# Performance work log

Hardware: AMD Instinct MI355X
Metric: run time of the kernel (lower is better)

The kernel has to match this reference:

```python
import jax, jax.numpy as jnp
import numpy as np

NP, P, H, NB = 14, 16, 12, 6  # n_patches per side, patch size, heads, blocks
HD, EMB, SEQ = 64, 768, NP * NP + 1


def _layernorm(x, g, b, eps=1e-5):
    m = x.mean(axis=-1, keepdims=True)
    v = x.var(axis=-1, keepdims=True)
    return (x - m) * jax.lax.rsqrt(v + eps) * g + b


def setup_inputs() -> dict:
    key = jax.random.key(0)
    ks = jax.random.split(key, 16)
    s = 0.02
    B = 64
    inp = {
        "images": jax.random.normal(ks[0], (B, 3, 224, 224), jnp.float32),
        "Wmap": jax.random.normal(ks[1], (768, 768), jnp.float32) * s,
        "bmap": jnp.zeros((768,), jnp.float32),
        "cls_tok": jax.random.normal(ks[2], (1, 768), jnp.float32) * s,
        "pos": jax.random.normal(ks[3], (SEQ, 768), jnp.float32) * s,
        "ln1_g": jnp.ones((NB, 768), jnp.float32),
        "ln1_b": jnp.zeros((NB, 768), jnp.float32),
        "Wq": jax.random.normal(ks[4], (NB, H, HD, HD), jnp.float32) * s,
        "bq": jnp.zeros((NB, H, HD), jnp.float32),
        "Wk": jax.random.normal(ks[5], (NB, H, HD, HD), jnp.float32) * s,
        "bk": jnp.zeros((NB, H, HD), jnp.float32),
        "Wv": jax.random.normal(ks[6], (NB, H, HD, HD), jnp.float32) * s,
        "bv": jnp.zeros((NB, H, HD), jnp.float32),
        "ln2_g": jnp.ones((NB, 768), jnp.float32),
        "ln2_b": jnp.zeros((NB, 768), jnp.float32),
        "W1": jax.random.normal(ks[7], (NB, 768, 3072), jnp.float32) * s,
        "b1": jnp.zeros((NB, 3072), jnp.float32),
        "W2": jax.random.normal(ks[8], (NB, 3072, 768), jnp.float32) * s,
        "b2": jnp.zeros((NB, 768), jnp.float32),
        "Whead": jax.random.normal(ks[9], (768, 10), jnp.float32) * s,
        "bhead": jnp.zeros((10,), jnp.float32),
    }
    return inp


def reference(images, Wmap, bmap, cls_tok, pos, ln1_g, ln1_b, Wq, bq, Wk, bk,
              Wv, bv, ln2_g, ln2_b, W1, b1, W2, b2, Whead, bhead):
    B = images.shape[0]
    # patchify: (B,3,224,224) -> (B,196,768); per-patch channel-first flatten
    x = images.reshape(B, 3, NP, P, NP, P)
    x = x.transpose(0, 2, 4, 1, 3, 5).reshape(B, NP * NP, 3 * P * P)
    tokens = x @ Wmap + bmap  # (B,196,768)
    tokens = jnp.concatenate(
        [jnp.broadcast_to(cls_tok[None], (B, 1, EMB)), tokens], axis=1)
    out = tokens + pos[None]  # (B,197,768)
    scale = 1.0 / jnp.sqrt(jnp.asarray(H, out.dtype))  # NOTE: source divides by sqrt(num_heads)
    for i in range(NB):
        h = _layernorm(out, ln1_g[i], ln1_b[i])
        xh = h.reshape(B, SEQ, H, HD)
        q = jnp.einsum('bshd,hde->bshe', xh, Wq[i]) + bq[i]
        k = jnp.einsum('bshd,hde->bshe', xh, Wk[i]) + bk[i]
        v = jnp.einsum('bshd,hde->bshe', xh, Wv[i]) + bv[i]
        attn = jax.nn.softmax(
            jnp.einsum('bqhd,bkhd->bhqk', q, k) * scale, axis=-1)
        o = jnp.einsum('bhqk,bkhd->bqhd', attn, v).reshape(B, SEQ, EMB)
        out = out + o
        h2 = _layernorm(out, ln2_g[i], ln2_b[i])
        mlp = jax.nn.gelu(h2 @ W1[i] + b1[i], approximate=False) @ W2[i] + b2[i]
        out = out + mlp
    cls = out[:, 0]  # (B,768)
    return jax.nn.softmax(cls @ Whead + bhead, axis=-1)
```

## Files before the change

### kernel.cpp

```cpp
#include <hip/hip_runtime.h>
#include <cstddef>

#define BATCH 64
#define SEQL  197
#define EMB   768
#define NH    12
#define HDIM  64
#define NBLK  6
#define MLPD  3072
#define TOKS  12608
#define PTOK  12544
#define ATT_SCALE 0.28867513459481287f
#define LOG2E 1.4426950408889634f

typedef short bf16x8 __attribute__((ext_vector_type(8)));
typedef float f32x4  __attribute__((ext_vector_type(4)));

__device__ inline float bf2f(unsigned short u) {
  union { unsigned int i; float f; } c; c.i = ((unsigned int)u) << 16; return c.f;
}
__device__ inline unsigned short f2bf(float f) {
  union { float f; unsigned int i; } c; c.f = f;
  unsigned int r = c.i + 0x7FFFu + ((c.i >> 16) & 1u);
  return (unsigned short)(r >> 16);
}

__device__ __forceinline__ float gelu_f(float x) {
  float u = __builtin_fabsf(x) * 0.70710678118654752f;
  float t = __builtin_amdgcn_rcpf(__builtin_fmaf(0.3275911f, u, 1.0f));
  float p = __builtin_fmaf(1.061405429f, t, -1.453152027f);
  p = __builtin_fmaf(p, t, 1.421413741f);
  p = __builtin_fmaf(p, t, -0.284496736f);
  p = __builtin_fmaf(p, t, 0.254829592f);
  p = p * t;
  float e = __expf(-u * u);
  float er = __builtin_fmaf(-p, e, 1.0f);
  er = __builtin_copysignf(er, x);
  return 0.5f * x * (1.0f + er);
}

__device__ __forceinline__ void gload16(const unsigned short* g, void* l) {
  __builtin_amdgcn_global_load_lds(
      (const __attribute__((address_space(1))) unsigned int*)g,
      (__attribute__((address_space(3))) unsigned int*)l, 16, 0, 0);
}

__global__ __launch_bounds__(256) void patchify_kernel(const float* __restrict__ img,
                                                       unsigned short* __restrict__ out) {
  int i4 = blockIdx.x * 256 + threadIdx.x;
  int f4 = i4 % 192;
  int r  = i4 / 192;
  int b  = r / 196, t = r - b * 196;
  int f  = f4 * 4;
  int c  = f >> 8;
  int rem = f & 255;
  int iy = rem >> 4, ix = rem & 15;
  int py = t / 14, px = t - py * 14;
  const float* src = img + ((((size_t)b * 3 + c) * 224 + py * 16 + iy) * 224 + px * 16 + ix);
  float4 v = *(const float4*)src;
  ushort4 u;
  u.x = f2bf(v.x); u.y = f2bf(v.y); u.z = f2bf(v.z); u.w = f2bf(v.w);
  *(ushort4*)(out + (size_t)r * 768 + f) = u;
}

__global__ __launch_bounds__(256) void clspos_kernel(const float* __restrict__ cls,
                                                     const float* __restrict__ pos,
                                                     float* __restrict__ X) {
  int idx = blockIdx.x * 256 + threadIdx.x;
  int b = idx / 768, e = idx - b * 768;
  X[(size_t)b * SEQL * 768 + e] = cls[e] + pos[e];
}

__global__ __launch_bounds__(256) void wconv_kernel(const float* __restrict__ W,
                                                    unsigned short* __restrict__ Wt,
                                                    int K, int N, int perm) {
  __shared__ float t[32][33];
  int k0 = blockIdx.x * 32, n0 = blockIdx.y * 32;
  int kk = threadIdx.x >> 3, nn = (threadIdx.x & 7) * 4;
  float4 v = *(const float4*)&W[(size_t)(k0 + kk) * N + n0 + nn];
  t[nn + 0][kk] = v.x; t[nn + 1][kk] = v.y; t[nn + 2][kk] = v.z; t[nn + 3][kk] = v.w;
  __syncthreads();
  int nr = threadIdx.x >> 3, kc = (threadIdx.x & 7) * 4;
  ushort4 u;
  u.x = f2bf(t[nr][kc + 0]); u.y = f2bf(t[nr][kc + 1]);
  u.z = f2bf(t[nr][kc + 2]); u.w = f2bf(t[nr][kc + 3]);
  if (!perm) {
    *(ushort4*)&Wt[(size_t)(n0 + nr) * K + k0 + kc] = u;
  } else {
    size_t base = (size_t)(n0 + nr) * K + (size_t)(k0 & ~63);
    int klo = (k0 & 32) + kc;
    size_t st = base + (size_t)((klo & 15) * 4 + (klo >> 4));
    Wt[st + 0]  = u.x;
    Wt[st + 4]  = u.y;
    Wt[st + 8]  = u.z;
    Wt[st + 12] = u.w;
  }
}

__global__ __launch_bounds__(256) void qwconv_kernel(const float* __restrict__ Wq,
                                                     const float* __restrict__ Wk,
                                                     const float* __restrict__ Wv,
                                                     unsigned short* __restrict__ Wt) {
  int mh = blockIdx.x;
  int m = mh / 12, h = mh - m * 12;
  const float* src = (m == 0 ? Wq : (m == 1 ? Wk : Wv)) + (size_t)h * 4096;
  unsigned short* dst = Wt + (size_t)mh * 4096;
  for (int idx = threadIdx.x; idx < 4096; idx += 256) {
    int d = idx >> 6, e = idx & 63;
    dst[e * 64 + d] = f2bf(src[idx]);
  }
}

template<int MODE>
__global__ __launch_bounds__(256) void gemm_mfma(const unsigned short* __restrict__ A, int lda,
                                                 const unsigned short* __restrict__ Bt, int ldb,
                                                 void* __restrict__ Cv,
                                                 const float* __restrict__ bias,
                                                 const float* __restrict__ pos,
                                                 int M, int N, int K) {
  __shared__ short As[8192];
  __shared__ short Bs[8192];
  const int tid  = threadIdx.x;
  const int wid  = tid >> 6, lane = tid & 63;
  const int wr   = wid >> 1, wc = wid & 1;
  const int fr   = lane & 15;
  const int fq   = lane >> 4;
  const int m0   = blockIdx.y * 128;
  const int n0   = blockIdx.x * 128;
  const int srow = lane >> 3;
  const int schk = lane & 7;
  const int Mc   = M - 1;

  const unsigned short* ap[4];
  const unsigned short* bp[4];
  char* al[4];
  char* bl[4];
#pragma unroll
  for (int i = 0; i < 4; ++i) {
    int row = i * 32 + wid * 8 + srow;
    int gr = m0 + row; if (gr > Mc) gr = Mc;
    int sw = (schk ^ (row & 7)) << 3;
    ap[i] = A + (size_t)gr * lda + sw;
    bp[i] = Bt + (size_t)(n0 + row) * ldb + sw;
    al[i] = (char*)As + i * 4096 + wid * 1024;
    bl[i] = (char*)Bs + i * 4096 + wid * 1024;
  }

  f32x4 acc[4][4];
#pragma unroll
  for (int m = 0; m < 4; ++m)
#pragma unroll
    for (int n = 0; n < 4; ++n) acc[m][n] = (f32x4)0.f;

  const int T = K >> 6;
  for (int t = 0; t < T; ++t) {
#pragma unroll
    for (int i = 0; i < 4; ++i) {
      gload16(ap[i], al[i]);
      gload16(bp[i], bl[i]);
      ap[i] += 64;
      bp[i] += 64;
    }
    __syncthreads();
#pragma unroll
    for (int ks = 0; ks < 2; ++ks) {
      bf16x8 af[4], bfr[4];
#pragma unroll
      for (int m = 0; m < 4; ++m) {
        int row = (wr << 6) + (m << 4) + fr;
        int ch = ((ks << 2) + fq) ^ (row & 7);
        af[m] = *(const bf16x8*)&As[(row << 6) + (ch << 3)];
      }
#pragma unroll
      for (int n = 0; n < 4; ++n) {
        int row = (wc << 6) + (n << 4) + fr;
        int ch = ((ks << 2) + fq) ^ (row & 7);
        bfr[n] = *(const bf16x8*)&Bs[(row << 6) + (ch << 3)];
      }
#pragma unroll
      for (int m = 0; m < 4; ++m)
#pragma unroll
        for (int n = 0; n < 4; ++n)
          acc[m][n] = __builtin_amdgcn_mfma_f32_16x16x32_bf16(af[m], bfr[n], acc[m][n], 0, 0, 0);
    }
    __syncthreads();
  }

#pragma unroll
  for (int m = 0; m < 4; ++m) {
#pragma unroll
    for (int j = 0; j < 4; ++j) {
      int r = m0 + (wr << 6) + (m << 4) + (fq << 2) + j;
      if (r >= M) continue;
      if (MODE == 1) {
        ushort4 q;
        float v0 = acc[m][0][j] + bias[n0 + (wc << 6) + 0 * 16 + fr];
        float v1 = acc[m][1][j] + bias[n0 + (wc << 6) + 1 * 16 + fr];
        float v2 = acc[m][2][j] + bias[n0 + (wc << 6) + 2 * 16 + fr];
        float v3 = acc[m][3][j] + bias[n0 + (wc << 6) + 3 * 16 + fr];
        q.x = f2bf(gelu_f(v0));
        q.y = f2bf(gelu_f(v1));
        q.z = f2bf(gelu_f(v2));
        q.w = f2bf(gelu_f(v3));
        *(ushort4*)&((unsigned short*)Cv)[(size_t)r * MLPD + n0 + (wc << 6) + fr * 4] = q;
      } else {
#pragma unroll
        for (int n = 0; n < 4; ++n) {
          int c = n0 + (wc << 6) + (n << 4) + fr;
          float v = acc[m][n][j] + bias[c];
          if (MODE == 0) {
            int b = r / 196, t = r - b * 196;
            ((float*)Cv)[((size_t)b * SEQL + 1 + t) * 768 + c] = v + pos[(size_t)(1 + t) * 768 + c];
          } else {
            ((float*)Cv)[(size_t)r * 768 + c] += v;
          }
        }
      }
    }
  }
}

__global__ __launch_bounds__(256) void ln_kernel(const float* __restrict__ Xi,
                                                 unsigned short* __restrict__ Ho,
                                                 const float* __restrict__ g,
                                                 const float* __restrict__ bb) {
  int tok = blockIdx.x * 4 + (threadIdx.x >> 6);
  int lane = threadIdx.x & 63;
  const float* x = Xi + (size_t)tok * 768;
  float4 v0 = *(const float4*)(x + lane * 4);
  float4 v1 = *(const float4*)(x + 256 + lane * 4);
  float4 v2 = *(const float4*)(x + 512 + lane * 4);
  float s = v0.x + v0.y + v0.z + v0.w + v1.x + v1.y + v1.z + v1.w + v2.x + v2.y + v2.z + v2.w;
  float q = v0.x*v0.x + v0.y*v0.y + v0.z*v0.z + v0.w*v0.w
          + v1.x*v1.x + v1.y*v1.y + v1.z*v1.z + v1.w*v1.w
          + v2.x*v2.x + v2.y*v2.y + v2.z*v2.z + v2.w*v2.w;
#pragma unroll
  for (int o = 32; o > 0; o >>= 1) { s += __shfl_xor(s, o); q += __shfl_xor(q, o); }
  float mean = s * (1.f / 768.f);
  float var  = q * (1.f / 768.f) - mean * mean;
  float rs = rsqrtf(var + 1e-5f);
  unsigned short* outp = Ho + (size_t)tok * 768;
  float4 g0 = *(const float4*)(g + lane * 4);
  float4 g1 = *(const float4*)(g + 256 + lane * 4);
  float4 g2 = *(const float4*)(g + 512 + lane * 4);
  float4 b0 = *(const float4*)(bb + lane * 4);
  float4 b1 = *(const float4*)(bb + 256 + lane * 4);
  float4 b2 = *(const float4*)(bb + 512 + lane * 4);
  ushort4 s0, s1, s2;
  s0.x = f2bf((v0.x - mean) * rs * g0.x + b0.x); s0.y = f2bf((v0.y - mean) * rs * g0.y + b0.y);
  s0.z = f2bf((v0.z - mean) * rs * g0.z + b0.z); s0.w = f2bf((v0.w - mean) * rs * g0.w + b0.w);
  s1.x = f2bf((v1.x - mean) * rs * g1.x + b1.x); s1.y = f2bf((v1.y - mean) * rs * g1.y + b1.y);
  s1.z = f2bf((v1.z - mean) * rs * g1.z + b1.z); s1.w = f2bf((v1.w - mean) * rs * g1.w + b1.w);
  s2.x = f2bf((v2.x - mean) * rs * g2.x + b2.x); s2.y = f2bf((v2.y - mean) * rs * g2.y + b2.y);
  s2.z = f2bf((v2.z - mean) * rs * g2.z + b2.z); s2.w = f2bf((v2.w - mean) * rs * g2.w + b2.w);
  *(ushort4*)(outp + lane * 4) = s0;
  *(ushort4*)(outp + 256 + lane * 4) = s1;
  *(ushort4*)(outp + 512 + lane * 4) = s2;
}

__global__ __launch_bounds__(256) void ln_res_kernel(float* __restrict__ X,
                                                     const unsigned short* __restrict__ O,
                                                     unsigned short* __restrict__ Ho,
                                                     const float* __restrict__ g,
                                                     const float* __restrict__ bb) {
  int tok = blockIdx.x * 4 + (threadIdx.x >> 6);
  int lane = threadIdx.x & 63;
  float* x = X + (size_t)tok * 768;
  const unsigned short* op = O + (size_t)tok * 768;
  float4 v0 = *(const float4*)(x + lane * 4);
  float4 v1 = *(const float4*)(x + 256 + lane * 4);
  float4 v2 = *(const float4*)(x + 512 + lane * 4);
  ushort4 o0 = *(const ushort4*)(op + lane * 4);
  ushort4 o1 = *(const ushort4*)(op + 256 + lane * 4);
  ushort4 o2 = *(const ushort4*)(op + 512 + lane * 4);
  v0.x += bf2f(o0.x); v0.y += bf2f(o0.y); v0.z += bf2f(o0.z); v0.w += bf2f(o0.w);
  v1.x += bf2f(o1.x); v1.y += bf2f(o1.y); v1.z += bf2f(o1.z); v1.w += bf2f(o1.w);
  v2.x += bf2f(o2.x); v2.y += bf2f(o2.y); v2.z += bf2f(o2.z); v2.w += bf2f(o2.w);
  *(float4*)(x + lane * 4) = v0;
  *(float4*)(x + 256 + lane * 4) = v1;
  *(float4*)(x + 512 + lane * 4) = v2;
  float s = v0.x + v0.y + v0.z + v0.w + v1.x + v1.y + v1.z + v1.w + v2.x + v2.y + v2.z + v2.w;
  float q = v0.x*v0.x + v0.y*v0.y + v0.z*v0.z + v0.w*v0.w
          + v1.x*v1.x + v1.y*v1.y + v1.z*v1.z + v1.w*v1.w
          + v2.x*v2.x + v2.y*v2.y + v2.z*v2.z + v2.w*v2.w;
#pragma unroll
  for (int o = 32; o > 0; o >>= 1) { s += __shfl_xor(s, o); q += __shfl_xor(q, o); }
  float mean = s * (1.f / 768.f);
  float var  = q * (1.f / 768.f) - mean * mean;
  float rs = rsqrtf(var + 1e-5f);
  unsigned short* outp = Ho + (size_t)tok * 768;
  float4 g0 = *(const float4*)(g + lane * 4);
  float4 g1 = *(const float4*)(g + 256 + lane * 4);
  float4 g2 = *(const float4*)(g + 512 + lane * 4);
  float4 b0 = *(const float4*)(bb + lane * 4);
  float4 b1 = *(const float4*)(bb + 256 + lane * 4);
  float4 b2 = *(const float4*)(bb + 512 + lane * 4);
  ushort4 s0, s1, s2;
  s0.x = f2bf((v0.x - mean) * rs * g0.x + b0.x); s0.y = f2bf((v0.y - mean) * rs * g0.y + b0.y);
  s0.z = f2bf((v0.z - mean) * rs * g0.z + b0.z); s0.w = f2bf((v0.w - mean) * rs * g0.w + b0.w);
  s1.x = f2bf((v1.x - mean) * rs * g1.x + b1.x); s1.y = f2bf((v1.y - mean) * rs * g1.y + b1.y);
  s1.z = f2bf((v1.z - mean) * rs * g1.z + b1.z); s1.w = f2bf((v1.w - mean) * rs * g1.w + b1.w);
  s2.x = f2bf((v2.x - mean) * rs * g2.x + b2.x); s2.y = f2bf((v2.y - mean) * rs * g2.y + b2.y);
  s2.z = f2bf((v2.z - mean) * rs * g2.z + b2.z); s2.w = f2bf((v2.w - mean) * rs * g2.w + b2.w);
  *(ushort4*)(outp + lane * 4) = s0;
  *(ushort4*)(outp + 256 + lane * 4) = s1;
  *(ushort4*)(outp + 512 + lane * 4) = s2;
}

__global__ __launch_bounds__(256) void qkv_mfma(const unsigned short* __restrict__ Hb,
    const unsigned short* __restrict__ Wt,
    const float* __restrict__ bq, const float* __restrict__ bk, const float* __restrict__ bv,
    unsigned short* __restrict__ Qo, unsigned short* __restrict__ Ko,
    unsigned short* __restrict__ Vo) {
  const int h = blockIdx.y;
  const int tid = threadIdx.x, wv = tid >> 6, lane = tid & 63;
  const int fr = lane & 15, hi = lane >> 4;
  const int t0 = blockIdx.x * 64 + wv * 16;
  const unsigned short* arow = Hb + (size_t)(t0 + fr) * 768 + h * 64;
  bf16x8 a0 = *(const bf16x8*)(arow + hi * 8);
  bf16x8 a1 = *(const bf16x8*)(arow + 32 + hi * 8);
  f32x4 acc[3][4];
#pragma unroll
  for (int m = 0; m < 3; ++m)
#pragma unroll
    for (int n = 0; n < 4; ++n) acc[m][n] = (f32x4)0.f;
#pragma unroll
  for (int m = 0; m < 3; ++m) {
    const unsigned short* wb = Wt + (size_t)(m * 12 + h) * 4096;
#pragma unroll
    for (int n = 0; n < 4; ++n) {
      bf16x8 b0 = *(const bf16x8*)&wb[(n * 16 + fr) * 64 + hi * 8];
      bf16x8 b1 = *(const bf16x8*)&wb[(n * 16 + fr) * 64 + 32 + hi * 8];
      acc[m][n] = __builtin_amdgcn_mfma_f32_16x16x32_bf16(a0, b0, acc[m][n], 0, 0, 0);
      acc[m][n] = __builtin_amdgcn_mfma_f32_16x16x32_bf16(a1, b1, acc[m][n], 0, 0, 0);
    }
  }
#pragma unroll
  for (int m = 0; m < 3; ++m) {
    const float* bptr = (m == 0 ? bq : (m == 1 ? bk : bv)) + h * 64;
    unsigned short* optr = (m == 0 ? Qo : (m == 1 ? Ko : Vo));
    const float sc = (m == 0) ? ATT_SCALE : 1.f;
#pragma unroll
    for (int j = 0; j < 4; ++j) {
      int tk = t0 + hi * 4 + j;
      int b = tk / 197, s = tk - b * 197;
      size_t base_o = (((size_t)b * NH + h) * SEQL + s) * 64;
      if (m < 2) {
        ushort4 o;
        o.x = f2bf((acc[m][0][j] + bptr[0 * 16 + fr]) * sc);
        o.y = f2bf((acc[m][1][j] + bptr[1 * 16 + fr]) * sc);
        o.z = f2bf((acc[m][2][j] + bptr[2 * 16 + fr]) * sc);
        o.w = f2bf((acc[m][3][j] + bptr[3 * 16 + fr]) * sc);
        *(ushort4*)&optr[base_o + fr * 4] = o;
      } else {
#pragma unroll
        for (int n = 0; n < 4; ++n)
          optr[base_o + n * 16 + fr] = f2bf(acc[m][n][j] + bptr[n * 16 + fr]);
      }
    }
  }
}

__global__ __launch_bounds__(256) void attn_kernel(const unsigned short* __restrict__ Q,
                                                   const unsigned short* __restrict__ Kg,
                                                   const unsigned short* __restrict__ Vg,
                                                   unsigned short* __restrict__ Ob) {
  __shared__ unsigned short Vt[64][200];
  __shared__ unsigned short Pl[4][16][200];
  const int bh = blockIdx.x;
  const int b = bh / NH, h = bh - b * NH;
  const int tid = threadIdx.x, wv = tid >> 6, lane = tid & 63;
  const int fr = lane & 15, hi = lane >> 4;
  const unsigned short* Qp = Q  + (size_t)bh * SEQL * 64;
  const unsigned short* Kp = Kg + (size_t)bh * SEQL * 64;
  const unsigned short* Vp = Vg + (size_t)bh * SEQL * 64;

  for (int idx = tid; idx < SEQL * 16; idx += 256) {
    int s = idx >> 4, d4 = (idx & 15) * 4;
    ushort4 v = *(const ushort4*)&Vp[s * 64 + d4];
    Vt[d4 + 0][s] = v.x; Vt[d4 + 1][s] = v.y; Vt[d4 + 2][s] = v.z; Vt[d4 + 3][s] = v.w;
  }
  __syncthreads();

  for (int qt = wv; qt < 13; qt += 4) {
    int qrow = qt * 16 + fr; if (qrow > 196) qrow = 196;
    bf16x8 qa0 = *(const bf16x8*)&Qp[qrow * 64 + hi * 8];
    bf16x8 qa1 = *(const bf16x8*)&Qp[qrow * 64 + 32 + hi * 8];
    f32x4 sc[13];
#pragma unroll
    for (int kt = 0; kt < 13; ++kt) {
      int krow = kt * 16 + fr; if (krow > 196) krow = 196;
      bf16x8 kb0 = *(const bf16x8*)&Kp[krow * 64 + hi * 8];
      bf16x8 kb1 = *(const bf16x8*)&Kp[krow * 64 + 32 + hi * 8];
      f32x4 a = (f32x4)0.f;
      a = __builtin_amdgcn_mfma_f32_16x16x32_bf16(qa0, kb0, a, 0, 0, 0);
      a = __builtin_amdgcn_mfma_f32_16x16x32_bf16(qa1, kb1, a, 0, 0, 0);
      sc[kt] = a;
    }
    float mx[4] = {-3e38f, -3e38f, -3e38f, -3e38f};
#pragma unroll
    for (int kt = 0; kt < 13; ++kt) {
      bool inval = (kt == 12) && (fr >= 5);
#pragma unroll
      for (int j = 0; j < 4; ++j) {
        float s = inval ? -3e38f : sc[kt][j];
        sc[kt][j] = s;
        mx[j] = fmaxf(mx[j], s);
      }
    }
#pragma unroll
    for (int o = 8; o > 0; o >>= 1)
#pragma unroll
      for (int j = 0; j < 4; ++j) mx[j] = fmaxf(mx[j], __shfl_xor(mx[j], o));
    float l[4] = {0.f, 0.f, 0.f, 0.f};
#pragma unroll
    for (int kt = 0; kt < 13; ++kt) {
      int col = kt * 16 + fr;
      bool storev = (col < 200);
#pragma unroll
      for (int j = 0; j < 4; ++j) {
        float p = exp2f((sc[kt][j] - mx[j]) * LOG2E);
        if ((kt == 12) && (fr >= 5)) p = 0.f;
        l[j] += p;
        if (storev) Pl[wv][hi * 4 + j][col] = f2bf(p);
      }
    }
#pragma unroll
    for (int o = 8; o > 0; o >>= 1)
#pragma unroll
      for (int j = 0; j < 4; ++j) l[j] += __shfl_xor(l[j], o);
    f32x4 ov[4];
#pragma unroll
    for (int n = 0; n < 4; ++n) ov[n] = (f32x4)0.f;
#pragma unroll
    for (int kc = 0; kc < 6; ++kc) {
      bf16x8 pa = *(const bf16x8*)&Pl[wv][fr][kc * 32 + hi * 8];
#pragma unroll
      for (int n = 0; n < 4; ++n) {
        bf16x8 vb = *(const bf16x8*)&Vt[n * 16 + fr][kc * 32 + hi * 8];
        ov[n] = __builtin_amdgcn_mfma_f32_16x16x32_bf16(pa, vb, ov[n], 0, 0, 0);
      }
    }
    {
      float pt[4][5];
#pragma unroll
      for (int j = 0; j < 4; ++j) {
        ushort4 p4 = *(ushort4*)&Pl[wv][hi * 4 + j][192];
        unsigned short p5 = Pl[wv][hi * 4 + j][196];
        pt[j][0] = bf2f(p4.x); pt[j][1] = bf2f(p4.y);
        pt[j][2] = bf2f(p4.z); pt[j][3] = bf2f(p4.w); pt[j][4] = bf2f(p5);
      }
#pragma unroll
      for (int n = 0; n < 4; ++n) {
        ushort4 v4 = *(ushort4*)&Vt[n * 16 + fr][192];
        unsigned short v5 = Vt[n * 16 + fr][196];
        float vt[5] = {bf2f(v4.x), bf2f(v4.y), bf2f(v4.z), bf2f(v4.w), bf2f(v5)};
#pragma unroll
        for (int j = 0; j < 4; ++j)
#pragma unroll
          for (int t = 0; t < 5; ++t)
            ov[n][j] = __builtin_fmaf(pt[j][t], vt[t], ov[n][j]);
      }
    }
#pragma unroll
    for (int j = 0; j < 4; ++j) {
      int r = qt * 16 + hi * 4 + j;
      if (r >= SEQL) continue;
      float inv = 1.f / l[j];
      unsigned short* op = Ob + ((size_t)b * SEQL + r) * 768 + h * 64 + fr;
#pragma unroll
      for (int n = 0; n < 4; ++n) op[n * 16] = f2bf(ov[n][j] * inv);
    }
  }
}

__global__ __launch_bounds__(64) void head_kernel(const float* __restrict__ X,
                                                  const float* __restrict__ Wh,
                                                  const float* __restrict__ bh,
                                                  float* __restrict__ out) {
  __shared__ float lg[10];
  int b = blockIdx.x, t = threadIdx.x;
  if (t < 10) {
    float acc = bh[t];
    const float* x = X + (size_t)b * SEQL * 768;
    for (int d = 0; d < 768; ++d) acc += x[d] * Wh[d * 10 + t];
    lg[t] = acc;
  }
  __syncthreads();
  if (t == 0) {
    float m = lg[0];
    for (int c = 1; c < 10; ++c) m = fmaxf(m, lg[c]);
    float ssum = 0.f;
    for (int c = 0; c < 10; ++c) ssum += expf(lg[c] - m);
    for (int c = 0; c < 10; ++c) out[b * 10 + c] = expf(lg[c] - m) / ssum;
  }
}

extern "C" void kernel_launch(void* const* d_in, const int* in_sizes, int n_in,
                              void* d_out, int out_size, void* d_ws, size_t ws_size,
                              hipStream_t stream) {
  const float* images = (const float*)d_in[0];
  const float* Wmap = (const float*)d_in[1];
  const float* bmap = (const float*)d_in[2];
  const float* cls  = (const float*)d_in[3];
  const float* pos  = (const float*)d_in[4];
  const float* ln1g = (const float*)d_in[5];
  const float* ln1b = (const float*)d_in[6];
  const float* Wq   = (const float*)d_in[7];
  const float* bq   = (const float*)d_in[8];
  const float* Wk   = (const float*)d_in[9];
  const float* bk   = (const float*)d_in[10];
  const float* Wv   = (const float*)d_in[11];
  const float* bv   = (const float*)d_in[12];
  const float* ln2g = (const float*)d_in[13];
  const float* ln2b = (const float*)d_in[14];
  const float* W1   = (const float*)d_in[15];
  const float* b1   = (const float*)d_in[16];
  const float* W2   = (const float*)d_in[17];
  const float* b2   = (const float*)d_in[18];
  const float* Wh   = (const float*)d_in[19];
  const float* bhd  = (const float*)d_in[20];
  float* out = (float*)d_out;

  const size_t ACT = (size_t)TOKS * 768;
  const size_t oX = 0;
  const size_t oHb = oX + ACT * 4;
  const size_t oR  = oHb + ACT * 2;
  const size_t oW1 = oR + 3 * ACT * 4;
  const size_t oW2 = oW1 + (size_t)768 * 3072 * 2;
  const size_t oWm = oW2 + (size_t)768 * 3072 * 2;
  const size_t oQW = oWm + (size_t)768 * 768 * 2;
  const size_t need = oQW + (size_t)36 * 4096 * 2;
  if (ws_size < need) return;

  char* ws = (char*)d_ws;
  float* X = (float*)(ws + oX);
  unsigned short* Hb = (unsigned short*)(ws + oHb);
  unsigned short* Qb = (unsigned short*)(ws + oR);
  unsigned short* Kb = Qb + ACT;
  unsigned short* Vb = Kb + ACT;
  unsigned short* mid = (unsigned short*)(ws + oR);
  unsigned short* Obuf = (unsigned short*)(ws + oR + 3 * ACT * 2);
  unsigned short* patches = (unsigned short*)(ws + oR);
  unsigned short* W1t = (unsigned short*)(ws + oW1);
  unsigned short* W2t = (unsigned short*)(ws + oW2);
  unsigned short* Wmapt = (unsigned short*)(ws + oWm);
  unsigned short* QWt = (unsigned short*)(ws + oQW);

  wconv_kernel<<<dim3(24, 24), 256, 0, stream>>>(Wmap, Wmapt, 768, 768, 0);
  patchify_kernel<<<9408, 256, 0, stream>>>(images, patches);
  clspos_kernel<<<192, 256, 0, stream>>>(cls, pos, X);
  gemm_mfma<0><<<dim3(6, 98), 256, 0, stream>>>(patches, 768, Wmapt, 768, X, bmap, pos,
                                                PTOK, 768, 768);

  for (int i = 0; i < NBLK; ++i) {
    ln_kernel<<<3152, 256, 0, stream>>>(X, Hb, ln1g + i * 768, ln1b + i * 768);
    qwconv_kernel<<<36, 256, 0, stream>>>(Wq + (size_t)i * 49152, Wk + (size_t)i * 49152,
                                          Wv + (size_t)i * 49152, QWt);
    qkv_mfma<<<dim3(197, 12), 256, 0, stream>>>(Hb, QWt,
        bq + i * 768, bk + i * 768, bv + i * 768, Qb, Kb, Vb);
    attn_kernel<<<768, 256, 0, stream>>>(Qb, Kb, Vb, Obuf);
    ln_res_kernel<<<3152, 256, 0, stream>>>(X, Obuf, Hb, ln2g + i * 768, ln2b + i * 768);
    wconv_kernel<<<dim3(24, 96), 256, 0, stream>>>(W1 + (size_t)i * 2359296, W1t, 768, MLPD, 0);
    wconv_kernel<<<dim3(96, 24), 256, 0, stream>>>(W2 + (size_t)i * 2359296, W2t, MLPD, 768, 1);
    gemm_mfma<1><<<dim3(24, 99), 256, 0, stream>>>(Hb, 768, W1t, 768, mid, b1 + i * MLPD,
                                                   nullptr, TOKS, MLPD, 768);
    gemm_mfma<2><<<dim3(6, 99), 256, 0, stream>>>(mid, MLPD, W2t, MLPD, X, b2 + i * 768,
                                                  nullptr, TOKS, 768, MLPD);
  }
  head_kernel<<<64, 64, 0, stream>>>(X, Wh, bhd, out);
}
```

Before: 1.926 ms.

## Add 256x256-tile 8-wave MFMA GEMM with XCD remap for MLP up-projection

Replaces the first MLP GEMM (768->3072 with GELU epilogue) with a new kernel that uses 256x256 output tiles, 512 threads, double-buffered swizzled LDS and direct global-to-LDS loads spread across MFMA phases. Workgroup indices are remapped so neighbouring tiles land on the same XCD for L2 reuse, and setprio is raised around MFMA bursts. The larger tiles cut operand reloads per FLOP, but they also lower occupancy (one block per CU) and leave some tail imbalance with 600 tiles.

```diff
diff --git a/kernel.cpp b/kernel.cpp
--- a/kernel.cpp
+++ b/kernel.cpp
@@ -216,6 +216,128 @@
           }
         }
       }
+    }
+  }
+}
+
+__global__ __launch_bounds__(512, 1) void gemm256p8(const unsigned short* __restrict__ A, int lda,
+                                                    const unsigned short* __restrict__ Bt, int ldb,
+                                                    unsigned short* __restrict__ Cv,
+                                                    const float* __restrict__ bias,
+                                                    int M, int K, int GX) {
+  __shared__ short As[2][16384];
+  __shared__ short Bs[2][16384];
+  const int nwg = gridDim.x;
+  const int orig = blockIdx.x;
+  const int qq = nwg >> 3, rr = nwg & 7, xcd = orig & 7, bidx = orig >> 3;
+  const int wg = (xcd < rr ? xcd * (qq + 1) : rr * (qq + 1) + (xcd - rr) * qq) + bidx;
+  const int m0 = (wg / GX) * 256;
+  const int n0 = (wg % GX) * 256;
+  const int tid = threadIdx.x;
+  const int wid = tid >> 6, lane = tid & 63;
+  const int wr = wid >> 2, wc = wid & 3;
+  const int fr = lane & 15, fq = lane >> 4, frk = fr & 7;
+  const int srow = lane >> 3, schk = lane & 7;
+  const int Mc = M - 1;
+  const int T = K >> 6;
+
+  const unsigned short* ap[4];
+  const unsigned short* bp[4];
+#pragma unroll
+  for (int p = 0; p < 4; ++p) {
+    int row = p * 64 + wid * 8 + srow;
+    int gr = m0 + row; if (gr > Mc) gr = Mc;
+    int sw = (schk ^ srow) << 3;
+    ap[p] = A + (size_t)gr * lda + sw;
+    bp[p] = Bt + (size_t)(n0 + row) * ldb + sw;
+  }
+
+  f32x4 acc[8][4];
+#pragma unroll
+  for (int m = 0; m < 8; ++m)
+#pragma unroll
+    for (int n = 0; n < 4; ++n) acc[m][n] = (f32x4)0.f;
+
+#pragma unroll
+  for (int p = 0; p < 4; ++p) {
+    gload16(ap[p], (char*)&As[0][0] + p * 8192 + wid * 1024);
+    gload16(bp[p], (char*)&Bs[0][0] + p * 8192 + wid * 1024);
+    ap[p] += 64; bp[p] += 64;
+  }
+
+  for (int t = 0; t < T; ++t) {
+    const int b = t & 1;
+    const bool st = (t + 1 < T);
+    asm volatile("s_waitcnt vmcnt(0)" ::: "memory");
+    __builtin_amdgcn_s_barrier();
+    const short* Ab = &As[b][0];
+    const short* Bb = &Bs[b][0];
+    char* Ad = (char*)&As[b ^ 1][0];
+    char* Bd = (char*)&Bs[b ^ 1][0];
+    bf16x8 bfv[4];
+#pragma unroll
+    for (int ph = 0; ph < 4; ++ph) {
+      const int ks = ph >> 1;
+      const int mg = ph & 1;
+      const int slot = ((ks << 2) + fq) ^ frk;
+      if (mg == 0) {
+#pragma unroll
+        for (int n = 0; n < 4; ++n) {
+          int row = wc * 64 + n * 16 + fr;
+          bfv[n] = *(const bf16x8*)&Bb[(row << 6) + (slot << 3)];
+        }
+      }
+      bf16x8 af[4];
+#pragma unroll
+      for (int mi = 0; mi < 4; ++mi) {
+        int row = wr * 128 + (mg * 4 + mi) * 16 + fr;
+        af[mi] = *(const bf16x8*)&Ab[(row << 6) + (slot << 3)];
+      }
+      if (st) {
+        if (ph == 0) {
+          gload16(ap[0], Ad + 0 * 8192 + wid * 1024); ap[0] += 64;
+          gload16(bp[0], Bd + 0 * 8192 + wid * 1024); bp[0] += 64;
+          gload16(ap[1], Ad + 1 * 8192 + wid * 1024); ap[1] += 64;
+          gload16(bp[1], Bd + 1 * 8192 + wid * 1024); bp[1] += 64;
+        } else if (ph == 1) {
+          gload16(ap[2], Ad + 2 * 8192 + wid * 1024); ap[2] += 64;
+          gload16(bp[2], Bd + 2 * 8192 + wid * 1024); bp[2] += 64;
+          gload16(ap[3], Ad + 3 * 8192 + wid * 1024); ap[3] += 64;
+          gload16(bp[3], Bd + 3 * 8192 + wid * 1024); bp[3] += 64;
+        }
+      }
+      __builtin_amdgcn_s_barrier();
+      asm volatile("s_waitcnt lgkmcnt(0)" ::: "memory");
+      __builtin_amdgcn_sched_barrier(0);
+      __builtin_amdgcn_s_setprio(1);
+#pragma unroll
+      for (int mi = 0; mi < 4; ++mi)
+#pragma unroll
+        for (int n = 0; n < 4; ++n)
+          acc[mg * 4 + mi][n] =
+              __builtin_amdgcn_mfma_f32_16x16x32_bf16(af[mi], bfv[n], acc[mg * 4 + mi][n], 0, 0, 0);
+      __builtin_amdgcn_s_setprio(0);
+      __builtin_amdgcn_sched_barrier(0);
+      __builtin_amdgcn_s_barrier();
+    }
+  }
+
+#pragma unroll
+  for (int m = 0; m < 8; ++m) {
+#pragma unroll
+    for (int j = 0; j < 4; ++j) {
+      int r = m0 + wr * 128 + m * 16 + (fq << 2) + j;
+      if (r >= M) continue;
+      float v0 = acc[m][0][j] + bias[n0 + wc * 64 + 0 * 16 + fr];
+      float v1 = acc[m][1][j] + bias[n0 + wc * 64 + 1 * 16 + fr];
+      float v2 = acc[m][2][j] + bias[n0 + wc * 64 + 2 * 16 + fr];
+      float v3 = acc[m][3][j] + bias[n0 + wc * 64 + 3 * 16 + fr];
+      ushort4 q;
+      q.x = f2bf(gelu_f(v0));
+      q.y = f2bf(gelu_f(v1));
+      q.z = f2bf(gelu_f(v2));
+      q.w = f2bf(gelu_f(v3));
+      *(ushort4*)&Cv[(size_t)r * MLPD + n0 + wc * 64 + fr * 4] = q;
     }
   }
 }
@@ -563,8 +685,8 @@
     ln_res_kernel<<<3152, 256, 0, stream>>>(X, Obuf, Hb, ln2g + i * 768, ln2b + i * 768);
     wconv_kernel<<<dim3(24, 96), 256, 0, stream>>>(W1 + (size_t)i * 2359296, W1t, 768, MLPD, 0);
     wconv_kernel<<<dim3(96, 24), 256, 0, stream>>>(W2 + (size_t)i * 2359296, W2t, MLPD, 768, 1);
-    gemm_mfma<1><<<dim3(24, 99), 256, 0, stream>>>(Hb, 768, W1t, 768, mid, b1 + i * MLPD,
-                                                   nullptr, TOKS, MLPD, 768);
+    gemm256p8<<<600, 512, 0, stream>>>(Hb, 768, W1t, 768, mid, b1 + i * MLPD,
+                                       TOKS, 768, 12);
     gemm_mfma<2><<<dim3(6, 99), 256, 0, stream>>>(mid, MLPD, W2t, MLPD, X, b2 + i * 768,
                                                   nullptr, TOKS, 768, MLPD);
   }
```

Measured after the change: 1.996 ms. 3.6% more time.
